# Performance work log

Hardware: AMD Instinct MI355X
Metric: run time of the kernel (lower is better)

Reference implementation:

```python
import jax, jax.numpy as jnp
import numpy as np

T, B, D, H, NQ = 512, 128, 512, 64, 64  # seq_len, batch, input_dim, hidden_dim == n_qubits
EPS = 1e-5

def setup_inputs() -> dict:
    key = jax.random.key(0)
    ks = jax.random.split(key, 11)
    s = 0.05
    return {
        "inputs": jax.random.normal(ks[0], (T, B, D), jnp.float32),
        "W0": jax.random.normal(ks[1], (4, NQ, D + H), jnp.float32) * s,
        "b0": jax.random.normal(ks[2], (4, NQ), jnp.float32) * s,
        "th0": jax.random.normal(ks[3], (4, NQ), jnp.float32) * s,
        "g0": jnp.ones((H,), jnp.float32),
        "be0": jnp.zeros((H,), jnp.float32),
        "W1": jax.random.normal(ks[4], (4, NQ, H + H), jnp.float32) * s,
        "b1": jax.random.normal(ks[5], (4, NQ), jnp.float32) * s,
        "th1": jax.random.normal(ks[6], (4, NQ), jnp.float32) * s,
        "g1": jnp.ones((H,), jnp.float32),
        "be1": jnp.zeros((H,), jnp.float32),
    }

def _qlstm_layer(x, W, b, th, gamma, beta):
    # x: [T, B, Din]. Faithful to source: h_prev = c_prev = 0 at EVERY timestep
    # (the torch code never writes back `states` inside the time loop), so all
    # timesteps are independent and fully vectorized.
    zeros_h = jnp.zeros(x.shape[:-1] + (H,), x.dtype)
    combined = jnp.concatenate([x, zeros_h], axis=-1)           # [T,B,Din+H]
    # 4 gate linears stacked on leading axis g: forget, input, update, output
    z = jnp.einsum('tbk,gnk->gtbn', combined, W) + b[:, None, None, :]
    # quantum circuit closed form: RX(z_i+th_i) per qubit + CNOT ladder + <Z_k>
    #   => cumprod_{i<=k} cos(z_i + th_i)
    q = jnp.cumprod(jnp.cos(z + th[:, None, None, :]), axis=-1)  # [4,T,B,NQ]
    sg = jax.nn.sigmoid(q)
    i_g = sg[1]
    g_g = jnp.tanh(sg[2])
    o_g = sg[3]
    # c = f * c_prev + i * g, with c_prev == 0  (f gate has no effect)
    c = i_g * g_g                                                # [T,B,H]
    h = o_g * jnp.tanh(c)
    mu = jnp.mean(h, axis=-1, keepdims=True)
    var = jnp.mean((h - mu) ** 2, axis=-1, keepdims=True)
    h_ln = (h - mu) * jax.lax.rsqrt(var + EPS) * gamma + beta
    return h_ln, c

def reference(inputs, W0, b0, th0, g0, be0, W1, b1, th1, g1, be1):
    h0, c0 = _qlstm_layer(inputs, W0, b0, th0, g0, be0)  # layer 0 (no dropout: p=0)
    h1, c1 = _qlstm_layer(h0, W1, b1, th1, g1, be1)      # layer 1
    outputs = h1                                          # [T,B,H]
    # new_states = states at the last timestep: [(h_ln, c)] per layer
    return (outputs, h0[-1], c0[-1], h1[-1], c1[-1])
```

## Files before the change

### kernel.cpp

```cpp
#include <hip/hip_runtime.h>
#include <hip/hip_bf16.h>

typedef __attribute__((ext_vector_type(8))) short bf16x8;
typedef __attribute__((ext_vector_type(4))) float f32x4;

#define T_SEQ   512
#define B_BATCH 128
#define H_DIM   64
#define MB      64
#define AS_STRIDE 136
#define ZS_STRIDE 193
#define HS_STRIDE 68
#define LASTROW ((T_SEQ - 1) * B_BATCH)

#define W0H 0
#define W0M 98304
#define W0L 196608
#define W1H 294912
#define W1M 307200
#define W1L 319488

__device__ __forceinline__ void tsplit(float f, unsigned& h, unsigned& m, unsigned& l) {
    unsigned uf = __builtin_bit_cast(unsigned, f);
    h = uf >> 16;
    float hf = __builtin_bit_cast(float, uf & 0xFFFF0000u);
    float r1 = f - hf;
    unsigned u1 = __builtin_bit_cast(unsigned, r1);
    m = u1 >> 16;
    float mf = __builtin_bit_cast(float, u1 & 0xFFFF0000u);
    float r2 = r1 - mf;
    l = __builtin_bit_cast(unsigned, r2) >> 16;
}

__device__ __forceinline__ void tsplit2(float a, float b,
                                        unsigned& ph, unsigned& pm, unsigned& pl) {
    unsigned ha, ma, la, hb, mb, lb;
    tsplit(a, ha, ma, la);
    tsplit(b, hb, mb, lb);
    ph = ha | (hb << 16);
    pm = ma | (mb << 16);
    pl = la | (lb << 16);
}

__device__ __forceinline__ f32x4 mfma6(bf16x8 ah, bf16x8 am, bf16x8 al,
                                       bf16x8 bh, bf16x8 bm, bf16x8 bl, f32x4 c) {
    c = __builtin_amdgcn_mfma_f32_16x16x32_bf16(ah, bh, c, 0, 0, 0);
    c = __builtin_amdgcn_mfma_f32_16x16x32_bf16(ah, bm, c, 0, 0, 0);
    c = __builtin_amdgcn_mfma_f32_16x16x32_bf16(am, bh, c, 0, 0, 0);
    c = __builtin_amdgcn_mfma_f32_16x16x32_bf16(ah, bl, c, 0, 0, 0);
    c = __builtin_amdgcn_mfma_f32_16x16x32_bf16(al, bh, c, 0, 0, 0);
    c = __builtin_amdgcn_mfma_f32_16x16x32_bf16(am, bm, c, 0, 0, 0);
    return c;
}

__device__ __forceinline__ float acc_sigmoid(float x) {
    float e = expf(-x);
    float d = 1.0f + e;
    float r = __builtin_amdgcn_rcpf(d);
    r = r * (2.0f - d * r);
    return r;
}

__global__ __launch_bounds__(256) void presplit_w(const float* __restrict__ W0,
                                                  const float* __restrict__ W1,
                                                  short* __restrict__ ws) {
    int i = blockIdx.x * 256 + threadIdx.x;
    if (i < 98304) {
        int r = i >> 9, k = i & 511;
        unsigned h, m, l;
        tsplit(W0[(r + 64) * 576 + k], h, m, l);
        ws[W0H + i] = (short)h;
        ws[W0M + i] = (short)m;
        ws[W0L + i] = (short)l;
    } else if (i < 110592) {
        int j = i - 98304;
        int r = j >> 6, k = j & 63;
        unsigned h, m, l;
        tsplit(W1[(r + 64) * 128 + k], h, m, l);
        ws[W1H + j] = (short)h;
        ws[W1M + j] = (short)m;
        ws[W1L + j] = (short)l;
    }
}

__global__ __launch_bounds__(256) void qlstm_fused(
    const float* __restrict__ x,
    const float* __restrict__ b0,
    const float* __restrict__ th0,
    const float* __restrict__ g0,
    const float* __restrict__ be0,
    const float* __restrict__ b1,
    const float* __restrict__ th1,
    const float* __restrict__ g1,
    const float* __restrict__ be1,
    const short* __restrict__ wsp,
    float* __restrict__ out)
{
    __shared__ __align__(16) char lds[71168];
    short* ah = (short*)lds;
    short* am = ah + 64 * AS_STRIDE;
    short* al = am + 64 * AS_STRIDE;
    float* zs  = (float*)lds;
    float* hs  = (float*)(lds + 52224);
    float* bt0 = (float*)(lds + 69632);
    float* bt1 = bt0 + 192;

    const int tid = threadIdx.x;
    const long rowbase = (long)blockIdx.x * MB;

    float* out0 = out;
    float* out1 = out + (long)T_SEQ * B_BATCH * H_DIM;
    float* out2 = out1 + B_BATCH * H_DIM;
    float* out3 = out2 + B_BATCH * H_DIM;
    float* out4 = out3 + B_BATCH * H_DIM;

    if (tid < 192) {
        bt0[tid] = b0[64 + tid] + th0[64 + tid];
        bt1[tid] = b1[64 + tid] + th1[64 + tid];
    }

    const int lane = tid & 63;
    const int wave = tid >> 6;
    const int ln   = lane & 15;
    const int quad = lane >> 4;
    const int cw   = wave * 48;

    int brow0[3], brow1[3];
    for (int nt = 0; nt < 3; ++nt) {
        int gc = cw + nt * 16 + ln;
        brow0[nt] = gc * 512;
        brow1[nt] = gc * 64;
    }

    f32x4 acc[4][3];
    for (int mt = 0; mt < 4; ++mt)
        for (int nt = 0; nt < 3; ++nt)
            acc[mt][nt] = (f32x4){0.f, 0.f, 0.f, 0.f};

    for (int kc = 0; kc < 512; kc += 128) {
        for (int pass = 0; pass < 4; ++pass) {
            int e  = pass * 256 + tid;
            int r  = e >> 4;
            int k8 = (e & 15) << 3;
            const float* xp = x + (rowbase + r) * 512 + kc + k8;
            float4 f0 = *(const float4*)xp;
            float4 f1 = *(const float4*)(xp + 4);
            uint4 Ph, Pm, Pl;
            tsplit2(f0.x, f0.y, Ph.x, Pm.x, Pl.x);
            tsplit2(f0.z, f0.w, Ph.y, Pm.y, Pl.y);
            tsplit2(f1.x, f1.y, Ph.z, Pm.z, Pl.z);
            tsplit2(f1.z, f1.w, Ph.w, Pm.w, Pl.w);
            int ao = r * AS_STRIDE + k8;
            *(uint4*)(ah + ao) = Ph;
            *(uint4*)(am + ao) = Pm;
            *(uint4*)(al + ao) = Pl;
        }
        __syncthreads();
        for (int k0 = 0; k0 < 128; k0 += 32) {
            int ka = k0 + quad * 8;
            bf16x8 Ah[4], Am[4], Al[4];
            for (int mt = 0; mt < 4; ++mt) {
                int ao = (mt * 16 + ln) * AS_STRIDE + ka;
                Ah[mt] = *(const bf16x8*)(ah + ao);
                Am[mt] = *(const bf16x8*)(am + ao);
                Al[mt] = *(const bf16x8*)(al + ao);
            }
            for (int nt = 0; nt < 3; ++nt) {
                int bo = brow0[nt] + kc + ka;
                bf16x8 Bh = *(const bf16x8*)(wsp + W0H + bo);
                bf16x8 Bm = *(const bf16x8*)(wsp + W0M + bo);
                bf16x8 Bl = *(const bf16x8*)(wsp + W0L + bo);
                for (int mt = 0; mt < 4; ++mt)
                    acc[mt][nt] = mfma6(Ah[mt], Am[mt], Al[mt], Bh, Bm, Bl, acc[mt][nt]);
            }
        }
        __syncthreads();
    }

    for (int mt = 0; mt < 4; ++mt)
        for (int nt = 0; nt < 3; ++nt)
            for (int i = 0; i < 4; ++i) {
                int row = mt * 16 + quad * 4 + i;
                int col = cw + nt * 16 + ln;
                zs[row * ZS_STRIDE + col] = acc[mt][nt][i];
            }
    __syncthreads();

    if (tid < 192) {
        int gi = tid >> 6;
        int r  = tid & 63;
        float* zrow = zs + r * ZS_STRIDE + gi * 64;
        const float* btg = bt0 + gi * 64;
        float p = 1.0f;
        for (int n = 0; n < 64; ++n) {
            p *= cosf(zrow[n] + btg[n]);
            zrow[n] = p;
        }
    }
    __syncthreads();

    {
        int r = tid >> 2;
        int j = tid & 3;
        long tbrow = rowbase + r;
        bool lastt = (tbrow >= LASTROW);
        int bidx = (int)(tbrow - LASTROW);
        const float* zr = zs + r * ZS_STRIDE;
        float h[16];
        float s = 0.f;
        for (int i = 0; i < 16; ++i) {
            int n = j * 16 + i;
            float q1 = zr[n];
            float q2 = zr[64 + n];
            float q3 = zr[128 + n];
            float ig = acc_sigmoid(q1);
            float gg = tanhf(acc_sigmoid(q2));
            float og = acc_sigmoid(q3);
            float c  = ig * gg;
            float hv = og * tanhf(c);
            h[i] = hv;
            s += hv;
            if (lastt) out2[bidx * 64 + n] = c;
        }
        s += __shfl_xor(s, 1);  s += __shfl_xor(s, 2);
        float mu = s * (1.0f / 64.0f);
        float s2 = 0.f;
        for (int i = 0; i < 16; ++i) {
            float d = h[i] - mu;
            s2 += d * d;
        }
        s2 += __shfl_xor(s2, 1); s2 += __shfl_xor(s2, 2);
        float var = s2 * (1.0f / 64.0f);
        float rs  = rsqrtf(var + 1e-5f);
        for (int i = 0; i < 16; ++i) {
            int n = j * 16 + i;
            float hl = (h[i] - mu) * rs * g0[n] + be0[n];
            hs[r * HS_STRIDE + n] = hl;
            if (lastt) out1[bidx * 64 + n] = hl;
        }
    }
    __syncthreads();

    f32x4 acc2[4][3];
    for (int mt = 0; mt < 4; ++mt)
        for (int nt = 0; nt < 3; ++nt)
            acc2[mt][nt] = (f32x4){0.f, 0.f, 0.f, 0.f};
    for (int k0 = 0; k0 < 64; k0 += 32) {
        int ka = k0 + quad * 8;
        bf16x8 Ah[4], Am[4], Al[4];
        for (int mt = 0; mt < 4; ++mt) {
            const float* p = hs + (mt * 16 + ln) * HS_STRIDE + ka;
            float4 f0 = *(const float4*)p;
            float4 f1 = *(const float4*)(p + 4);
            uint4 Ph, Pm, Pl;
            tsplit2(f0.x, f0.y, Ph.x, Pm.x, Pl.x);
            tsplit2(f0.z, f0.w, Ph.y, Pm.y, Pl.y);
            tsplit2(f1.x, f1.y, Ph.z, Pm.z, Pl.z);
            tsplit2(f1.z, f1.w, Ph.w, Pm.w, Pl.w);
            Ah[mt] = __builtin_bit_cast(bf16x8, Ph);
            Am[mt] = __builtin_bit_cast(bf16x8, Pm);
            Al[mt] = __builtin_bit_cast(bf16x8, Pl);
        }
        for (int nt = 0; nt < 3; ++nt) {
            int bo = brow1[nt] + ka;
            bf16x8 Bh = *(const bf16x8*)(wsp + W1H + bo);
            bf16x8 Bm = *(const bf16x8*)(wsp + W1M + bo);
            bf16x8 Bl = *(const bf16x8*)(wsp + W1L + bo);
            for (int mt = 0; mt < 4; ++mt)
                acc2[mt][nt] = mfma6(Ah[mt], Am[mt], Al[mt], Bh, Bm, Bl, acc2[mt][nt]);
        }
    }
    for (int mt = 0; mt < 4; ++mt)
        for (int nt = 0; nt < 3; ++nt)
            for (int i = 0; i < 4; ++i) {
                int row = mt * 16 + quad * 4 + i;
                int col = cw + nt * 16 + ln;
                zs[row * ZS_STRIDE + col] = acc2[mt][nt][i];
            }
    __syncthreads();

    if (tid < 192) {
        int gi = tid >> 6;
        int r  = tid & 63;
        float* zrow = zs + r * ZS_STRIDE + gi * 64;
        const float* btg = bt1 + gi * 64;
        float p = 1.0f;
        for (int n = 0; n < 64; ++n) {
            p *= cosf(zrow[n] + btg[n]);
            zrow[n] = p;
        }
    }
    __syncthreads();

    {
        int r = tid >> 2;
        int j = tid & 3;
        long tbrow = rowbase + r;
        bool lastt = (tbrow >= LASTROW);
        int bidx = (int)(tbrow - LASTROW);
        const float* zr = zs + r * ZS_STRIDE;
        float h[16];
        float s = 0.f;
        for (int i = 0; i < 16; ++i) {
            int n = j * 16 + i;
            float q1 = zr[n];
            float q2 = zr[64 + n];
            float q3 = zr[128 + n];
            float ig = acc_sigmoid(q1);
            float gg = tanhf(acc_sigmoid(q2));
            float og = acc_sigmoid(q3);
            float c  = ig * gg;
            float hv = og * tanhf(c);
            h[i] = hv;
            s += hv;
            if (lastt) out4[bidx * 64 + n] = c;
        }
        s += __shfl_xor(s, 1);  s += __shfl_xor(s, 2);
        float mu = s * (1.0f / 64.0f);
        float s2 = 0.f;
        for (int i = 0; i < 16; ++i) {
            float d = h[i] - mu;
            s2 += d * d;
        }
        s2 += __shfl_xor(s2, 1); s2 += __shfl_xor(s2, 2);
        float var = s2 * (1.0f / 64.0f);
        float rs  = rsqrtf(var + 1e-5f);
        float o4[16];
        for (int i = 0; i < 16; ++i)
            o4[i] = (h[i] - mu) * rs * g1[j * 16 + i] + be1[j * 16 + i];
        float* dst = out0 + tbrow * 64 + j * 16;
        for (int i4 = 0; i4 < 4; ++i4)
            *(float4*)(dst + i4 * 4) = *(float4*)(o4 + i4 * 4);
        if (lastt) {
            float* dst3 = out3 + (long)bidx * 64 + j * 16;
            for (int i4 = 0; i4 < 4; ++i4)
                *(float4*)(dst3 + i4 * 4) = *(float4*)(o4 + i4 * 4);
        }
    }
}

extern "C" void kernel_launch(void* const* d_in, const int* in_sizes, int n_in,
                              void* d_out, int out_size, void* d_ws, size_t ws_size,
                              hipStream_t stream) {
    const float* x   = (const float*)d_in[0];
    const float* W0  = (const float*)d_in[1];
    const float* b0  = (const float*)d_in[2];
    const float* th0 = (const float*)d_in[3];
    const float* g0  = (const float*)d_in[4];
    const float* be0 = (const float*)d_in[5];
    const float* W1  = (const float*)d_in[6];
    const float* b1  = (const float*)d_in[7];
    const float* th1 = (const float*)d_in[8];
    const float* g1  = (const float*)d_in[9];
    const float* be1 = (const float*)d_in[10];
    short* wsp = (short*)d_ws;

    presplit_w<<<dim3(432), dim3(256), 0, stream>>>(W0, W1, wsp);
    qlstm_fused<<<dim3(1024), dim3(256), 0, stream>>>(
        x, b0, th0, g0, be0, b1, th1, g1, be1, wsp, (float*)d_out);
}
```

Before: 329.0 us.

## Use fast cos/sigmoid/tanh, pre-split layer-1 activations into LDS, shrink LDS for occupancy

Swaps cosf, expf and tanhf for inline polynomial and exp/rcp approximations in the gate and cumprod paths. The layer-1 activations are now split into three bf16 parts once and stored in LDS, so the MFMA loop loads them directly instead of re-splitting fp32 per tile. This lets the hidden-state buffer share the aliased LDS region, which shrinks shared memory and adds a launch-bounds occupancy hint of 3 blocks per CU. Extra barriers are added to protect the aliased region, and the approximations may differ slightly in accuracy from the library calls.

```diff
diff --git a/kernel.cpp b/kernel.cpp
--- a/kernel.cpp
+++ b/kernel.cpp
@@ -10,7 +10,7 @@
 #define MB      64
 #define AS_STRIDE 136
 #define ZS_STRIDE 193
-#define HS_STRIDE 68
+#define A2S       72
 #define LASTROW ((T_SEQ - 1) * B_BATCH)
 
 #define W0H 0
@@ -53,12 +53,39 @@
     return c;
 }
 
-__device__ __forceinline__ float acc_sigmoid(float x) {
-    float e = expf(-x);
+__device__ __forceinline__ float fast_cos(float x) {
+    float n = rintf(x * 0.6366197723675814f);
+    int   m = (int)n;
+    float r = __builtin_fmaf(n, -1.5707962512969971e+00f, x);
+    r = __builtin_fmaf(n, -7.5497894158615964e-08f, r);
+    r = __builtin_fmaf(n, -5.3903025299577647e-15f, r);
+    float r2 = r * r;
+    float ps = __builtin_fmaf(r2, 2.7557314297e-06f, -1.9841270114e-04f);
+    ps = __builtin_fmaf(r2, ps, 8.3333337680e-03f);
+    ps = __builtin_fmaf(r2, ps, -1.6666667163e-01f);
+    float s = __builtin_fmaf(r * r2, ps, r);
+    float pc = __builtin_fmaf(r2, 2.4801587642e-05f, -1.3888889225e-03f);
+    pc = __builtin_fmaf(r2, pc, 4.1666667908e-02f);
+    pc = __builtin_fmaf(r2, pc, -0.5f);
+    float c = __builtin_fmaf(r2, pc, 1.0f);
+    float v = (m & 1) ? s : c;
+    unsigned sign = (unsigned)((m + 1) & 2) << 30;
+    return __builtin_bit_cast(float, __builtin_bit_cast(unsigned, v) ^ sign);
+}
+
+__device__ __forceinline__ float fast_sigmoid(float x) {
+    float e = __expf(-x);
     float d = 1.0f + e;
     float r = __builtin_amdgcn_rcpf(d);
+    return r * (2.0f - d * r);
+}
+
+__device__ __forceinline__ float fast_tanh_pos(float x) {
+    float t = __expf(2.0f * x);
+    float d = t + 1.0f;
+    float r = __builtin_amdgcn_rcpf(d);
     r = r * (2.0f - d * r);
-    return r;
+    return (t - 1.0f) * r;
 }
 
 __global__ __launch_bounds__(256) void presplit_w(const float* __restrict__ W0,
@@ -83,7 +110,7 @@
     }
 }
 
-__global__ __launch_bounds__(256) void qlstm_fused(
+__global__ __launch_bounds__(256, 3) void qlstm_fused(
     const float* __restrict__ x,
     const float* __restrict__ b0,
     const float* __restrict__ th0,
@@ -96,13 +123,15 @@
     const short* __restrict__ wsp,
     float* __restrict__ out)
 {
-    __shared__ __align__(16) char lds[71168];
+    __shared__ __align__(16) char lds[53760];
     short* ah = (short*)lds;
     short* am = ah + 64 * AS_STRIDE;
     short* al = am + 64 * AS_STRIDE;
     float* zs  = (float*)lds;
-    float* hs  = (float*)(lds + 52224);
-    float* bt0 = (float*)(lds + 69632);
+    short* a2h = (short*)lds;
+    short* a2m = a2h + 64 * A2S;
+    short* a2l = a2m + 64 * A2S;
+    float* bt0 = (float*)(lds + 52224);
     float* bt1 = bt0 + 192;
 
     const int tid = threadIdx.x;
@@ -193,7 +222,7 @@
         const float* btg = bt0 + gi * 64;
         float p = 1.0f;
         for (int n = 0; n < 64; ++n) {
-            p *= cosf(zrow[n] + btg[n]);
+            p *= fast_cos(zrow[n] + btg[n]);
             zrow[n] = p;
         }
     }
@@ -213,11 +242,11 @@
             float q1 = zr[n];
             float q2 = zr[64 + n];
             float q3 = zr[128 + n];
-            float ig = acc_sigmoid(q1);
-            float gg = tanhf(acc_sigmoid(q2));
-            float og = acc_sigmoid(q3);
+            float ig = fast_sigmoid(q1);
+            float gg = fast_tanh_pos(fast_sigmoid(q2));
+            float og = fast_sigmoid(q3);
             float c  = ig * gg;
-            float hv = og * tanhf(c);
+            float hv = og * fast_tanh_pos(c);
             h[i] = hv;
             s += hv;
             if (lastt) out2[bidx * 64 + n] = c;
@@ -232,12 +261,30 @@
         s2 += __shfl_xor(s2, 1); s2 += __shfl_xor(s2, 2);
         float var = s2 * (1.0f / 64.0f);
         float rs  = rsqrtf(var + 1e-5f);
+        float hl[16];
         for (int i = 0; i < 16; ++i) {
             int n = j * 16 + i;
-            float hl = (h[i] - mu) * rs * g0[n] + be0[n];
-            hs[r * HS_STRIDE + n] = hl;
-            if (lastt) out1[bidx * 64 + n] = hl;
-        }
+            hl[i] = (h[i] - mu) * rs * g0[n] + be0[n];
+            if (lastt) out1[bidx * 64 + n] = hl[i];
+        }
+        __syncthreads();
+
+        int ab = r * A2S + j * 16;
+        uint4 Ph, Pm, Pl;
+        tsplit2(hl[0], hl[1], Ph.x, Pm.x, Pl.x);
+        tsplit2(hl[2], hl[3], Ph.y, Pm.y, Pl.y);
+        tsplit2(hl[4], hl[5], Ph.z, Pm.z, Pl.z);
+        tsplit2(hl[6], hl[7], Ph.w, Pm.w, Pl.w);
+        *(uint4*)(a2h + ab) = Ph;
+        *(uint4*)(a2m + ab) = Pm;
+        *(uint4*)(a2l + ab) = Pl;
+        tsplit2(hl[8],  hl[9],  Ph.x, Pm.x, Pl.x);
+        tsplit2(hl[10], hl[11], Ph.y, Pm.y, Pl.y);
+        tsplit2(hl[12], hl[13], Ph.z, Pm.z, Pl.z);
+        tsplit2(hl[14], hl[15], Ph.w, Pm.w, Pl.w);
+        *(uint4*)(a2h + ab + 8) = Ph;
+        *(uint4*)(a2m + ab + 8) = Pm;
+        *(uint4*)(a2l + ab + 8) = Pl;
     }
     __syncthreads();
 
@@ -249,17 +296,10 @@
         int ka = k0 + quad * 8;
         bf16x8 Ah[4], Am[4], Al[4];
         for (int mt = 0; mt < 4; ++mt) {
-            const float* p = hs + (mt * 16 + ln) * HS_STRIDE + ka;
-            float4 f0 = *(const float4*)p;
-            float4 f1 = *(const float4*)(p + 4);
-            uint4 Ph, Pm, Pl;
-            tsplit2(f0.x, f0.y, Ph.x, Pm.x, Pl.x);
-            tsplit2(f0.z, f0.w, Ph.y, Pm.y, Pl.y);
-            tsplit2(f1.x, f1.y, Ph.z, Pm.z, Pl.z);
-            tsplit2(f1.z, f1.w, Ph.w, Pm.w, Pl.w);
-            Ah[mt] = __builtin_bit_cast(bf16x8, Ph);
-            Am[mt] = __builtin_bit_cast(bf16x8, Pm);
-            Al[mt] = __builtin_bit_cast(bf16x8, Pl);
+            int ao = (mt * 16 + ln) * A2S + ka;
+            Ah[mt] = *(const bf16x8*)(a2h + ao);
+            Am[mt] = *(const bf16x8*)(a2m + ao);
+            Al[mt] = *(const bf16x8*)(a2l + ao);
         }
         for (int nt = 0; nt < 3; ++nt) {
             int bo = brow1[nt] + ka;
@@ -270,6 +310,7 @@
                 acc2[mt][nt] = mfma6(Ah[mt], Am[mt], Al[mt], Bh, Bm, Bl, acc2[mt][nt]);
         }
     }
+    __syncthreads();
     for (int mt = 0; mt < 4; ++mt)
         for (int nt = 0; nt < 3; ++nt)
             for (int i = 0; i < 4; ++i) {
@@ -286,7 +327,7 @@
         const float* btg = bt1 + gi * 64;
         float p = 1.0f;
         for (int n = 0; n < 64; ++n) {
-            p *= cosf(zrow[n] + btg[n]);
+            p *= fast_cos(zrow[n] + btg[n]);
             zrow[n] = p;
         }
     }
@@ -306,11 +347,11 @@
             float q1 = zr[n];
             float q2 = zr[64 + n];
             float q3 = zr[128 + n];
-            float ig = acc_sigmoid(q1);
-            float gg = tanhf(acc_sigmoid(q2));
-            float og = acc_sigmoid(q3);
+            float ig = fast_sigmoid(q1);
+            float gg = fast_tanh_pos(fast_sigmoid(q2));
+            float og = fast_sigmoid(q3);
             float c  = ig * gg;
-            float hv = og * tanhf(c);
+            float hv = og * fast_tanh_pos(c);
             h[i] = hv;
             s += hv;
             if (lastt) out4[bidx * 64 + n] = c;
```

New measurement: 323.2 us. No clear change (-1.7%).
